# Optimization experiments

Hardware: AMD Instinct MI355X
Metric: run time of the kernel (lower is better)

## Reference

```python
import jax, jax.numpy as jnp
import numpy as np

THRESHOLD = 0.05
TOP_N = 512
NMS_THR = 0.6
POST_TOP_N = 100
MIN_SIZE = 0.0
N_CLASS = 8
IMG_SIZE = (256.0, 256.0, 64.0)
B, C, H, W, D = 4, 8, 128, 128, 32


def _pairwise_iou3d(b):
    # b: [K, 6] in xyzxyz; returns [K, K] volumetric IoU
    lo, hi = b[:, :3], b[:, 3:]
    ilo = jnp.maximum(lo[:, None, :], lo[None, :, :])
    ihi = jnp.minimum(hi[:, None, :], hi[None, :, :])
    inter = jnp.prod(jnp.maximum(ihi - ilo, 0.0), axis=-1)
    vol = jnp.prod(jnp.maximum(hi - lo, 0.0), axis=-1)
    return inter / (vol[:, None] + vol[None, :] - inter + 1e-9)


def _nms_keep(boxes, scores, thr):
    # greedy NMS; scores == -1 marks invalid entries. Returns bool keep mask [K].
    K = boxes.shape[0]
    order = jnp.argsort(-scores)
    b = boxes[order]
    s = scores[order]
    iou = _pairwise_iou3d(b)
    idx = jnp.arange(K)

    def body(i, keep):
        sup = (iou[i] > thr) & keep[i] & (idx > i)
        return keep & ~sup

    keep = jax.lax.fori_loop(0, K, body, s > 0.0)
    return jnp.zeros(K, dtype=bool).at[order].set(keep)


def _forward(location, cls_pred, box_pred, center_pred):
    Bb, Cc = cls_pred.shape[0], cls_pred.shape[1]
    N = cls_pred.shape[2] * cls_pred.shape[3] * cls_pred.shape[4]
    # [B, C, H, W, D] -> [B, N, C]
    cls = jax.nn.sigmoid(cls_pred).transpose(0, 2, 3, 4, 1).reshape(Bb, N, Cc)
    ctr = jax.nn.sigmoid(center_pred).transpose(0, 2, 3, 4, 1).reshape(Bb, N)
    box = box_pred.transpose(0, 2, 3, 4, 1).reshape(Bb, N, 6)

    candid = cls > THRESHOLD                      # [B, N, C]
    scores = cls * ctr[:, :, None]                # centerness-weighted
    flat = jnp.where(candid, scores, -1.0).reshape(Bb, N * Cc)
    vals, idx = jax.lax.top_k(flat, TOP_N)        # fixed-size stand-in for mask+topk
    valid = vals > 0.0                            # matches torch clamp(count, top_n)

    loc_idx = idx // Cc                           # flattened spatial location
    class_id = idx % Cc + 1                       # labels are 1-based
    bsel = jnp.take_along_axis(box, loc_idx[..., None], axis=1)   # [B, K, 6]
    lsel = location[loc_idx]                                      # [B, K, 3]
    det = jnp.concatenate([lsel - bsel[..., :3], lsel + bsel[..., 3:]], axis=-1)

    # BoxList.clip to image volume
    full = jnp.concatenate([jnp.asarray(IMG_SIZE), jnp.asarray(IMG_SIZE)]).astype(det.dtype) - 1.0
    det = jnp.clip(det, 0.0, full)

    score = jnp.where(valid, jnp.sqrt(jnp.where(valid, vals, 1.0)), 0.0)

    # remove_small_boxes
    sides = det[..., 3:] - det[..., :3]
    valid = valid & jnp.all(sides >= MIN_SIZE, axis=-1)

    # per-class greedy NMS (decisions are non-differentiable; torch detaches anyway)
    det_ng = jax.lax.stop_gradient(det)
    score_ng = jax.lax.stop_gradient(score)

    def per_image(b_i, s_i, c_i, v_i):
        def per_class(j):
            m = v_i & (c_i == j)
            return _nms_keep(b_i, jnp.where(m, s_i, -1.0), NMS_THR) & m
        return jnp.any(jax.vmap(per_class)(jnp.arange(1, N_CLASS + 1)), axis=0)

    valid = jax.vmap(per_image)(det_ng, score_ng, class_id, valid)

    # post_top_n selection (kthvalue threshold == keep top post_top_n scores)
    fv, fi = jax.lax.top_k(jnp.where(valid, score_ng, -1.0), POST_TOP_N)
    fvalid = fv > 0.0
    fbox = jnp.take_along_axis(det, fi[..., None], axis=1) * fvalid[..., None]
    fscore = jnp.where(fvalid, jnp.take_along_axis(score, fi, axis=1), 0.0)
    flabel = jnp.where(fvalid, jnp.take_along_axis(class_id, fi, axis=1), 0)
    return fbox, fscore, flabel, fvalid


def setup_inputs() -> dict:
    key = jax.random.key(0)
    k1, k2, k3, k4 = jax.random.split(key, 4)
    N = H * W * D
    location = jax.random.uniform(k1, (N, 3), dtype=jnp.float32) * jnp.asarray(IMG_SIZE, jnp.float32)
    cls_pred = jax.random.normal(k2, (B, C, H, W, D), dtype=jnp.float32) - 2.0  # realistic logits
    box_pred = jax.random.uniform(k3, (B, 6, H, W, D), dtype=jnp.float32) * 20.0  # positive extents
    center_pred = jax.random.normal(k4, (B, 1, H, W, D), dtype=jnp.float32)
    return {"location": location, "cls_pred": cls_pred, "box_pred": box_pred, "center_pred": center_pred}


def reference(location, cls_pred, box_pred, center_pred):
    return _forward(location, cls_pred, box_pred, center_pred)
```

## Files before the change

kernel.cpp:

```cpp
#include <hip/hip_runtime.h>

#define NB 4
#define NC 8
#define NLOC 524288
#define TOPN 512
#define POST 100
#define NBIN 8192
#define SELBINS 4096
#define SCAP 4096
#define CAP 16384
#define KPT 16
#define LCAP 2048
#define NMS_THR 0.6f
#define CAND_THR 0.05f
#define SPEC_THR 0.5f

typedef unsigned long long ull;

#define OFF_CNT    0
#define OFF_OVF    16
#define OFF_KEYS   64
#define ZERO_BYTES 32

__device__ __forceinline__ float sigmoidf_(float x) {
    return 1.0f / (1.0f + __expf(-x));
}

__global__ __launch_bounds__(256) void gather_spec(const float* __restrict__ cls,
                                                   const float* __restrict__ ctr,
                                                   ull* __restrict__ keys,
                                                   unsigned int* __restrict__ counts,
                                                   unsigned int* __restrict__ ovf) {
    __shared__ ull lkeys[LCAP];
    __shared__ unsigned int lcnt;
    __shared__ unsigned int lbase;
    const int b = blockIdx.y;
    if (threadIdx.x == 0) lcnt = 0;
    __syncthreads();

    const int n0 = (blockIdx.x * blockDim.x + threadIdx.x) * 8;
    const float4* cvp = (const float4*)(ctr + (size_t)b * NLOC + n0);
    const float4 cv0 = cvp[0], cv1 = cvp[1];
    float4 cl0[NC], cl1[NC];
    #pragma unroll
    for (int c = 0; c < NC; ++c) {
        const float4* p = (const float4*)(cls + ((size_t)b * NC + c) * NLOC + n0);
        cl0[c] = p[0];
        cl1[c] = p[1];
    }

    #pragma unroll
    for (int h = 0; h < 2; ++h) {
        const float4 cv = h ? cv1 : cv0;
        #pragma unroll
        for (int j = 0; j < 4; ++j) {
            bool any = false;
            #pragma unroll
            for (int c = 0; c < NC; ++c) {
                const float x = h ? ((const float*)&cl1[c])[j] : ((const float*)&cl0[c])[j];
                any |= (x > 0.0f);
            }
            if (any) {
                const float sc = sigmoidf_(((const float*)&cv)[j]);
                #pragma unroll
                for (int c = 0; c < NC; ++c) {
                    const float x = h ? ((const float*)&cl1[c])[j] : ((const float*)&cl0[c])[j];
                    if (x > 0.0f) {
                        const float p = sigmoidf_(x) * sc;
                        if (p > SPEC_THR) {
                            const unsigned pos = atomicAdd(&lcnt, 1u);
                            if (pos < LCAP) {
                                const unsigned flat = (unsigned)((n0 + h * 4 + j) * NC + c);
                                lkeys[pos] = ((ull)__float_as_uint(p) << 32) | (unsigned)(~flat);
                            }
                        }
                    }
                }
            }
        }
    }
    __syncthreads();
    const unsigned m = lcnt;
    if (threadIdx.x == 0) {
        const unsigned stored = (m > LCAP) ? LCAP : m;
        lbase = atomicAdd(&counts[b], stored);
        if (m > LCAP) ovf[b] = 1;
    }
    __syncthreads();
    const unsigned stored = (m > LCAP) ? LCAP : m;
    const unsigned base = lbase;
    for (unsigned i = threadIdx.x; i < stored; i += blockDim.x) {
        const unsigned pos = base + i;
        if (pos < CAP) keys[(size_t)b * CAP + pos] = lkeys[i];
    }
}

__device__ __forceinline__ float iou3d_(const float* a, const float* bx) {
    const float ix = fminf(a[3], bx[3]) - fmaxf(a[0], bx[0]);
    const float iy = fminf(a[4], bx[4]) - fmaxf(a[1], bx[1]);
    const float iz = fminf(a[5], bx[5]) - fmaxf(a[2], bx[2]);
    const float inter = fmaxf(ix, 0.0f) * fmaxf(iy, 0.0f) * fmaxf(iz, 0.0f);
    const float v0 = fmaxf(a[3] - a[0], 0.0f) * fmaxf(a[4] - a[1], 0.0f) * fmaxf(a[5] - a[2], 0.0f);
    const float v1 = fmaxf(bx[3] - bx[0], 0.0f) * fmaxf(bx[4] - bx[1], 0.0f) * fmaxf(bx[5] - bx[2], 0.0f);
    return inter / (v0 + v1 - inter + 1e-9f);
}

__global__ __launch_bounds__(1024) void select_nms_kernel(const float* __restrict__ cls,
                                                          const float* __restrict__ ctr,
                                                          ull* __restrict__ keys,
                                                          unsigned int* __restrict__ counts,
                                                          const unsigned int* __restrict__ ovf,
                                                          const float* __restrict__ loc,
                                                          const float* __restrict__ box,
                                                          float* __restrict__ out) {
    __shared__ union SU {
        struct { unsigned int hist[SELBINS]; ull surv[SCAP]; } sel;
        unsigned int fhist[NBIN];
        struct { float sd[TOPN * 6]; float ss[TOPN]; int scl[TOPN];
                 int keep[TOPN]; int clist[NC][TOPN];
                 float cbox[NC][128][6]; int wcnt[NC]; } nms;
    } u;
    __shared__ ull tk[TOPN];
    __shared__ unsigned int scnt;
    __shared__ int cut_s;

    const int b = blockIdx.x, t = threadIdx.x;
    const int lane = t & 63;

    {
        const unsigned cnt0 = counts[b];
        const bool bad = !(cnt0 >= TOPN && cnt0 <= CAP && ovf[b] == 0);
        if (bad) {
            for (int i = t; i < NBIN; i += 1024) u.fhist[i] = 0;
            __syncthreads();
            for (int n = t; n < NLOC; n += 1024) {
                const float sc = sigmoidf_(ctr[(size_t)b * NLOC + n]);
                #pragma unroll
                for (int c = 0; c < NC; ++c) {
                    const float s = sigmoidf_(cls[((size_t)b * NC + c) * NLOC + n]);
                    if (s > CAND_THR) atomicAdd(&u.fhist[__float_as_uint(s * sc) >> 17], 1u);
                }
            }
            __syncthreads();
            if (t == 0) {
                unsigned cum = 0; int bin = 0;
                for (int i = NBIN - 1; i >= 0; --i) {
                    cum += u.fhist[i];
                    if (cum >= TOPN) { bin = i; break; }
                }
                cut_s = bin;
                counts[b] = 0;
            }
            __syncthreads();
            const unsigned cb2 = (unsigned)cut_s;
            for (int n = t; n < NLOC; n += 1024) {
                const float sc = sigmoidf_(ctr[(size_t)b * NLOC + n]);
                #pragma unroll
                for (int c = 0; c < NC; ++c) {
                    const float s = sigmoidf_(cls[((size_t)b * NC + c) * NLOC + n]);
                    if (s > CAND_THR) {
                        const unsigned bits = __float_as_uint(s * sc);
                        if ((bits >> 17) >= cb2) {
                            const unsigned pos = atomicAdd(&counts[b], 1u);
                            if (pos < CAP)
                                keys[(size_t)b * CAP + pos] =
                                    ((ull)bits << 32) | (unsigned)(~(unsigned)(n * NC + c));
                        }
                    }
                }
            }
            __threadfence();
        }
    }
    __syncthreads();

    const int M = (int)min(counts[b], (unsigned)CAP);

    ull kr[KPT];
    {
        const ulonglong2* kb = (const ulonglong2*)(keys + (size_t)b * CAP);
        #pragma unroll
        for (int p = 0; p < KPT / 2; ++p) {
            const int vi = p * 1024 + t;
            ulonglong2 v; v.x = 0; v.y = 0;
            if (2 * vi < M) v = kb[vi];
            kr[2 * p] = v.x;
            kr[2 * p + 1] = v.y;
        }
    }

    for (int i = t; i < SELBINS; i += 1024) u.sel.hist[i] = 0;
    if (t == 0) scnt = 0;
    __syncthreads();
    #pragma unroll
    for (int p = 0; p < KPT / 2; ++p) {
        #pragma unroll
        for (int q = 0; q < 2; ++q) {
            const int i = 2 * (p * 1024 + t) + q;
            if (i < M) {
                const unsigned hi = (unsigned)(kr[2 * p + q] >> 32);
                const int off = (int)hi - 0x3F000000;
                int bin = (off < 0) ? 0 : (off >> 11);
                if (bin > SELBINS - 1) bin = SELBINS - 1;
                atomicAdd(&u.sel.hist[bin], 1u);
            }
        }
    }
    __syncthreads();

    if (t < 64) {
        unsigned s = 0;
        #pragma unroll 8
        for (int i = 0; i < 64; ++i)
            s += u.sel.hist[t * 64 + ((i + t) & 63)];
        unsigned suf = s;
        #pragma unroll
        for (int d = 1; d < 64; d <<= 1) {
            const unsigned o = __shfl_down(suf, d);
            suf += (t + d < 64) ? o : 0u;
        }
        const ull mask = __ballot(suf >= TOPN);
        unsigned nxt = __shfl_down(suf, 1);
        if (t == 63) nxt = 0;
        if (mask == 0ull) {
            if (t == 0) cut_s = 0;
        } else {
            const int L = 63 - __builtin_clzll(mask);
            if (t == L) {
                unsigned cum = nxt;
                int c = L * 64;
                for (int i = 63; i >= 0; --i) {
                    cum += u.sel.hist[L * 64 + i];
                    if (cum >= TOPN) { c = L * 64 + i; break; }
                }
                cut_s = c;
            }
        }
    }
    __syncthreads();

    const int cb = cut_s;
    #pragma unroll
    for (int p = 0; p < KPT / 2; ++p) {
        #pragma unroll
        for (int q = 0; q < 2; ++q) {
            const int i = 2 * (p * 1024 + t) + q;
            const ull k = kr[2 * p + q];
            bool pred = false;
            if (i < M) {
                const unsigned hi = (unsigned)(k >> 32);
                const int off = (int)hi - 0x3F000000;
                int bin = (off < 0) ? 0 : (off >> 11);
                if (bin > SELBINS - 1) bin = SELBINS - 1;
                pred = (bin >= cb);
            }
            const ull mv = __ballot(pred);
            unsigned base = 0;
            if (lane == 0 && mv) base = atomicAdd(&scnt, (unsigned)__popcll(mv));
            base = __shfl(base, 0);
            if (pred) {
                const unsigned pos = base + (unsigned)__popcll(mv & ((1ull << lane) - 1ull));
                if (pos < SCAP) u.sel.surv[pos] = k;
            }
        }
    }
    __syncthreads();

    const unsigned sc_final = scnt;
    if (sc_final <= (unsigned)SCAP) {
        const int S = (int)sc_final;
        for (int i = t; i < S; i += 1024) {
            const ull ke = u.sel.surv[i];
            int r = 0;
            int j = 0;
            for (; j + 16 <= S; j += 16) {
                #pragma unroll
                for (int qq = 0; qq < 16; ++qq) r += (u.sel.surv[j + qq] > ke) ? 1 : 0;
            }
            for (; j < S; ++j) r += (u.sel.surv[j] > ke) ? 1 : 0;
            if (r < TOPN) tk[r] = ke;
        }
        for (int r = S + t; r < TOPN; r += 1024) tk[r] = 0;
    } else {
        for (int i = t; i < M; i += 1024) {
            const ull ke = keys[(size_t)b * CAP + i];
            int r = 0;
            for (int j = 0; j < M; ++j) r += (keys[(size_t)b * CAP + j] > ke) ? 1 : 0;
            if (r < TOPN) tk[r] = ke;
        }
        const int W = (M < TOPN) ? M : TOPN;
        for (int r = W + t; r < TOPN; r += 1024) tk[r] = 0;
    }
    __syncthreads();

    if (t < TOPN) {
        const ull k = tk[t];
        const unsigned bits = (unsigned)(k >> 32);
        const float val = __uint_as_float(bits);
        int valid = (val > 0.0f) ? 1 : 0;
        const unsigned flat = ~(unsigned)(k & 0xffffffffu);
        int n = 0, c = 0;
        if (valid) { n = (int)(flat >> 3); c = (int)(flat & 7u); }
        const float lx = loc[n * 3 + 0], ly = loc[n * 3 + 1], lz = loc[n * 3 + 2];
        const float* bp = box + (size_t)b * 6 * NLOC + n;
        const float b0 = bp[0];
        const float b1 = bp[(size_t)NLOC];
        const float b2 = bp[2 * (size_t)NLOC];
        const float b3 = bp[3 * (size_t)NLOC];
        const float b4 = bp[4 * (size_t)NLOC];
        const float b5 = bp[5 * (size_t)NLOC];
        const float d0 = fminf(fmaxf(lx - b0, 0.0f), 255.0f);
        const float d1 = fminf(fmaxf(ly - b1, 0.0f), 255.0f);
        const float d2 = fminf(fmaxf(lz - b2, 0.0f), 63.0f);
        const float d3 = fminf(fmaxf(lx + b3, 0.0f), 255.0f);
        const float d4 = fminf(fmaxf(ly + b4, 0.0f), 255.0f);
        const float d5 = fminf(fmaxf(lz + b5, 0.0f), 63.0f);
        if (d3 - d0 < 0.0f || d4 - d1 < 0.0f || d5 - d2 < 0.0f) valid = 0;
        u.nms.sd[t * 6 + 0] = d0; u.nms.sd[t * 6 + 1] = d1; u.nms.sd[t * 6 + 2] = d2;
        u.nms.sd[t * 6 + 3] = d3; u.nms.sd[t * 6 + 4] = d4; u.nms.sd[t * 6 + 5] = d5;
        u.nms.ss[t] = (val > 0.0f) ? sqrtf(val) : 0.0f;
        u.nms.scl[t] = c + 1;
        u.nms.keep[t] = valid;
    }
    __syncthreads();

    if (t < TOPN) {
        const int w = t >> 6;
        const int myclass = w + 1;
        int cnt = 0;
        for (int j0 = 0; j0 < TOPN; j0 += 64) {
            const int j = j0 + lane;
            const bool pred = (u.nms.scl[j] == myclass) && (u.nms.keep[j] != 0);
            const ull m = __ballot(pred);
            if (pred) {
                const int pos = cnt + __popcll(m & ((1ull << lane) - 1ull));
                u.nms.clist[w][pos] = j;
                if (pos < 128) {
                    #pragma unroll
                    for (int q = 0; q < 6; ++q) u.nms.cbox[w][pos][q] = u.nms.sd[j * 6 + q];
                }
            }
            cnt += __popcll(m);
        }
        __threadfence_block();

        if (cnt <= 128) {
            const bool h0 = (lane < cnt), h1 = (lane + 64 < cnt);
            float A0[6], A1[6];
            #pragma unroll
            for (int q = 0; q < 6; ++q) {
                A0[q] = h0 ? u.nms.cbox[w][lane][q] : 0.0f;
                A1[q] = h1 ? u.nms.cbox[w][lane + 64][q] : 0.0f;
            }
            ull s0 = 0, s1lo = 0, s1hi = 0;
            #pragma unroll 2
            for (int i = 0; i < cnt; ++i) {
                float pb[6];
                #pragma unroll
                for (int q = 0; q < 6; ++q) pb[q] = u.nms.cbox[w][i][q];
                if (i < 64) {
                    if (h0 && lane > i && iou3d_(A0, pb) > NMS_THR) s0 |= 1ull << i;
                    if (h1 && iou3d_(A1, pb) > NMS_THR) s1lo |= 1ull << i;
                } else {
                    if (h1 && (i - 64) < lane && iou3d_(A1, pb) > NMS_THR) s1hi |= 1ull << (i - 64);
                }
            }
            bool a0 = h0, a1 = h1;
            ull m0 = __ballot(a0), m1 = __ballot(a1);
            for (int i = 0; i < cnt; ++i) {
                const bool alive_i = (i < 64) ? ((m0 >> i) & 1ull) : ((m1 >> (i - 64)) & 1ull);
                if (!alive_i) continue;
                if (a0 && i < 64 && ((s0 >> i) & 1ull)) a0 = false;
                if (a1) {
                    const bool sb = (i < 64) ? ((s1lo >> i) & 1ull) : ((s1hi >> (i - 64)) & 1ull);
                    if (sb) a1 = false;
                }
                m0 = __ballot(a0); m1 = __ballot(a1);
            }
            if (h0 && !a0) u.nms.keep[u.nms.clist[w][lane]] = 0;
            if (h1 && !a1) u.nms.keep[u.nms.clist[w][lane + 64]] = 0;
        } else {
            volatile int* vkeep = u.nms.keep;
            for (int i = 0; i < cnt; ++i) {
                const int gi = u.nms.clist[w][i];
                if (!vkeep[gi]) continue;
                float pb[6];
                #pragma unroll
                for (int q = 0; q < 6; ++q) pb[q] = u.nms.sd[gi * 6 + q];
                for (int e = i + 1 + lane; e < cnt; e += 64) {
                    const int gj = u.nms.clist[w][e];
                    if (vkeep[gj]) {
                        float cb_[6];
                        #pragma unroll
                        for (int q = 0; q < 6; ++q) cb_[q] = u.nms.sd[gj * 6 + q];
                        if (iou3d_(cb_, pb) > NMS_THR) vkeep[gj] = 0;
                    }
                }
                __threadfence_block();
            }
        }
    }
    __syncthreads();

    if (t < TOPN) {
        const int w = t >> 6;
        const ull km = __ballot(u.nms.keep[t] != 0);
        if (lane == 0) u.nms.wcnt[w] = __popcll(km);
    }
    __syncthreads();
    if (t < TOPN) {
        const int w = t >> 6;
        const ull km = __ballot(u.nms.keep[t] != 0);
        int before = 0, total = 0;
        #pragma unroll
        for (int w2 = 0; w2 < NC; ++w2) {
            total += u.nms.wcnt[w2];
            if (w2 < w) before += u.nms.wcnt[w2];
        }
        const int myrank = before + __popcll(km & ((1ull << lane) - 1ull));

        float* fbox = out;
        float* fscore = out + NB * POST * 6;
        float* flabel = out + NB * POST * 7;
        float* fvalid = out + NB * POST * 8;

        if (u.nms.keep[t] && myrank < POST) {
            #pragma unroll
            for (int k = 0; k < 6; ++k) fbox[(b * POST + myrank) * 6 + k] = u.nms.sd[t * 6 + k];
            fscore[b * POST + myrank] = u.nms.ss[t];
            flabel[b * POST + myrank] = (float)u.nms.scl[t];
            fvalid[b * POST + myrank] = 1.0f;
        }
        const int tc = (total < POST) ? total : POST;
        if (t >= tc && t < POST) {
            #pragma unroll
            for (int k = 0; k < 6; ++k) fbox[(b * POST + t) * 6 + k] = 0.0f;
            fscore[b * POST + t] = 0.0f;
            flabel[b * POST + t] = 0.0f;
            fvalid[b * POST + t] = 0.0f;
        }
    }
}

extern "C" void kernel_launch(void* const* d_in, const int* in_sizes, int n_in,
                              void* d_out, int out_size, void* d_ws, size_t ws_size,
                              hipStream_t stream) {
    const float* location = (const float*)d_in[0];
    const float* cls_pred = (const float*)d_in[1];
    const float* box_pred = (const float*)d_in[2];
    const float* ctr_pred = (const float*)d_in[3];

    char* ws = (char*)d_ws;
    unsigned int* counts = (unsigned int*)(ws + OFF_CNT);
    unsigned int* ovf    = (unsigned int*)(ws + OFF_OVF);
    ull*          keys   = (ull*)(ws + OFF_KEYS);

    hipMemsetAsync(d_ws, 0, ZERO_BYTES, stream);

    gather_spec<<<dim3(NLOC / 2048, NB), 256, 0, stream>>>(cls_pred, ctr_pred, keys, counts, ovf);
    select_nms_kernel<<<NB, 1024, 0, stream>>>(cls_pred, ctr_pred, keys, counts, ovf,
                                               location, box_pred, (float*)d_out);
}
```

Baseline: 88.24 us.

## Replace global atomic key append with per-block slots and bisection threshold select

```diff
diff --git a/kernel.cpp b/kernel.cpp
--- a/kernel.cpp
+++ b/kernel.cpp
@@ -6,21 +6,22 @@
 #define TOPN 512
 #define POST 100
 #define NBIN 8192
-#define SELBINS 4096
-#define SCAP 4096
-#define CAP 16384
-#define KPT 16
-#define LCAP 2048
+#define SLOTS 256
+#define SLOTW 128
+#define KEYSPAN (SLOTS*SLOTW)
+#define FB_CAP 16384
+#define SCAP 1024
+#define KPT 32
+#define LCAP 256
 #define NMS_THR 0.6f
 #define CAND_THR 0.05f
 #define SPEC_THR 0.5f
 
 typedef unsigned long long ull;
 
-#define OFF_CNT    0
-#define OFF_OVF    16
-#define OFF_KEYS   64
-#define ZERO_BYTES 32
+#define OFF_CNT  0
+#define OFF_OVF  4096
+#define OFF_KEYS 8192
 
 __device__ __forceinline__ float sigmoidf_(float x) {
     return 1.0f / (1.0f + __expf(-x));
@@ -29,11 +30,10 @@
 __global__ __launch_bounds__(256) void gather_spec(const float* __restrict__ cls,
                                                    const float* __restrict__ ctr,
                                                    ull* __restrict__ keys,
-                                                   unsigned int* __restrict__ counts,
-                                                   unsigned int* __restrict__ ovf) {
+                                                   unsigned int* __restrict__ cnt_arr,
+                                                   unsigned int* __restrict__ ovf_arr) {
     __shared__ ull lkeys[LCAP];
     __shared__ unsigned int lcnt;
-    __shared__ unsigned int lbase;
     const int b = blockIdx.y;
     if (threadIdx.x == 0) lcnt = 0;
     __syncthreads();
@@ -81,17 +81,91 @@
     }
     __syncthreads();
     const unsigned m = lcnt;
+    const unsigned stored = (m > (unsigned)SLOTW) ? (unsigned)SLOTW : m;
+    ull* kb = keys + ((size_t)b * SLOTS + blockIdx.x) * SLOTW;
+    for (unsigned i = threadIdx.x; i < stored; i += blockDim.x) kb[i] = lkeys[i];
     if (threadIdx.x == 0) {
-        const unsigned stored = (m > LCAP) ? LCAP : m;
-        lbase = atomicAdd(&counts[b], stored);
-        if (m > LCAP) ovf[b] = 1;
-    }
-    __syncthreads();
-    const unsigned stored = (m > LCAP) ? LCAP : m;
-    const unsigned base = lbase;
-    for (unsigned i = threadIdx.x; i < stored; i += blockDim.x) {
-        const unsigned pos = base + i;
-        if (pos < CAP) keys[(size_t)b * CAP + pos] = lkeys[i];
+        cnt_arr[b * SLOTS + blockIdx.x] = stored;
+        ovf_arr[b * SLOTS + blockIdx.x] = (m > (unsigned)SLOTW) ? 1u : 0u;
+    }
+}
+
+__global__ __launch_bounds__(1024) void fallback_kernel(const float* __restrict__ cls,
+                                                        const float* __restrict__ ctr,
+                                                        ull* __restrict__ keys,
+                                                        unsigned int* __restrict__ cnt_arr,
+                                                        unsigned int* __restrict__ ovf_arr) {
+    __shared__ unsigned red[32];
+    __shared__ int bad_s;
+    __shared__ unsigned hist[NBIN];
+    __shared__ unsigned cut_s, lpos;
+    const int b = blockIdx.x, t = threadIdx.x;
+
+    unsigned c = 0, o = 0;
+    if (t < SLOTS) { c = cnt_arr[b * SLOTS + t]; o = ovf_arr[b * SLOTS + t]; }
+    #pragma unroll
+    for (int d = 32; d >= 1; d >>= 1) { c += __shfl_down(c, d); o |= __shfl_down(o, d); }
+    if ((t & 63) == 0 && t < SLOTS) { red[t >> 6] = c; red[16 + (t >> 6)] = o; }
+    __syncthreads();
+    if (t == 0) {
+        const unsigned tot = red[0] + red[1] + red[2] + red[3];
+        const unsigned ov = red[16] | red[17] | red[18] | red[19];
+        bad_s = (tot < (unsigned)TOPN) || (ov != 0u);
+    }
+    __syncthreads();
+    if (!bad_s) return;
+
+    for (int i = t; i < NBIN; i += 1024) hist[i] = 0;
+    if (t == 0) lpos = 0;
+    __syncthreads();
+    for (int n = t; n < NLOC; n += 1024) {
+        const float scv = sigmoidf_(ctr[(size_t)b * NLOC + n]);
+        #pragma unroll
+        for (int cc = 0; cc < NC; ++cc) {
+            const float x = cls[((size_t)b * NC + cc) * NLOC + n];
+            if (x > -2.9444390f) {
+                const float s = sigmoidf_(x);
+                if (s > CAND_THR) atomicAdd(&hist[__float_as_uint(s * scv) >> 17], 1u);
+            }
+        }
+    }
+    __syncthreads();
+    if (t == 0) {
+        unsigned cum = 0; unsigned bin = 0;
+        for (int i = NBIN - 1; i >= 0; --i) {
+            cum += hist[i];
+            if (cum >= (unsigned)TOPN) { bin = (unsigned)i; break; }
+        }
+        cut_s = bin;
+    }
+    __syncthreads();
+    const unsigned cb = cut_s;
+    for (int n = t; n < NLOC; n += 1024) {
+        const float scv = sigmoidf_(ctr[(size_t)b * NLOC + n]);
+        #pragma unroll
+        for (int cc = 0; cc < NC; ++cc) {
+            const float x = cls[((size_t)b * NC + cc) * NLOC + n];
+            if (x > -2.9444390f) {
+                const float s = sigmoidf_(x);
+                if (s > CAND_THR) {
+                    const unsigned bits = __float_as_uint(s * scv);
+                    if ((bits >> 17) >= cb) {
+                        const unsigned pos = atomicAdd(&lpos, 1u);
+                        if (pos < (unsigned)FB_CAP)
+                            keys[(size_t)b * KEYSPAN + pos] =
+                                ((ull)bits << 32) | (unsigned)(~(unsigned)(n * NC + cc));
+                    }
+                }
+            }
+        }
+    }
+    __syncthreads();
+    const int M_fb = (int)((lpos < (unsigned)FB_CAP) ? lpos : (unsigned)FB_CAP);
+    if (t < SLOTS) {
+        int rem = M_fb - t * SLOTW;
+        rem = (rem < 0) ? 0 : ((rem > SLOTW) ? SLOTW : rem);
+        cnt_arr[b * SLOTS + t] = (unsigned)rem;
+        ovf_arr[b * SLOTS + t] = 0u;
     }
 }
 
@@ -105,191 +179,132 @@
     return inter / (v0 + v1 - inter + 1e-9f);
 }
 
-__global__ __launch_bounds__(1024) void select_nms_kernel(const float* __restrict__ cls,
-                                                          const float* __restrict__ ctr,
-                                                          ull* __restrict__ keys,
-                                                          unsigned int* __restrict__ counts,
-                                                          const unsigned int* __restrict__ ovf,
+__global__ __launch_bounds__(1024) void select_nms_kernel(const ull* __restrict__ keys,
+                                                          const unsigned int* __restrict__ cnt_arr,
                                                           const float* __restrict__ loc,
                                                           const float* __restrict__ box,
                                                           float* __restrict__ out) {
-    __shared__ union SU {
-        struct { unsigned int hist[SELBINS]; ull surv[SCAP]; } sel;
-        unsigned int fhist[NBIN];
-        struct { float sd[TOPN * 6]; float ss[TOPN]; int scl[TOPN];
-                 int keep[TOPN]; int clist[NC][TOPN];
-                 float cbox[NC][128][6]; int wcnt[NC]; } nms;
-    } u;
+    __shared__ union { ull surv[SCAP]; int clist[NC][TOPN]; } u;
     __shared__ ull tk[TOPN];
-    __shared__ unsigned int scnt;
-    __shared__ int cut_s;
+    __shared__ float sd[TOPN * 6];
+    __shared__ float ss[TOPN];
+    __shared__ int scl[TOPN];
+    __shared__ int keep[TOPN];
+    __shared__ float cbox[NC][SLOTW][6];
+    __shared__ int wcnt[NC];
+    __shared__ unsigned lcnt256[SLOTS];
+    __shared__ unsigned wred[32];
+    __shared__ unsigned scnt;
 
     const int b = blockIdx.x, t = threadIdx.x;
-    const int lane = t & 63;
-
-    {
-        const unsigned cnt0 = counts[b];
-        const bool bad = !(cnt0 >= TOPN && cnt0 <= CAP && ovf[b] == 0);
-        if (bad) {
-            for (int i = t; i < NBIN; i += 1024) u.fhist[i] = 0;
+    const int lane = t & 63, wid = t >> 6;
+
+    if (t < SLOTS) lcnt256[t] = cnt_arr[b * SLOTS + t];
+    __syncthreads();
+
+    const ull* kb = keys + (size_t)b * KEYSPAN;
+    ull kv[KPT];
+    #pragma unroll
+    for (int j = 0; j < KPT; ++j) {
+        const int g = j * 1024 + t;
+        const ull v = kb[g];
+        kv[j] = (((unsigned)g & (SLOTW - 1)) < lcnt256[g >> 7]) ? v : 0ull;
+    }
+
+    unsigned lo = 0u, hb = 0x7F800000u;
+    int it = 0;
+    while (lo < hb) {
+        const unsigned mid = (lo + hb) >> 1;
+        unsigned c = 0;
+        #pragma unroll
+        for (int j = 0; j < KPT; ++j) c += ((unsigned)(kv[j] >> 32) > mid) ? 1u : 0u;
+        #pragma unroll
+        for (int d = 32; d >= 1; d >>= 1) c += __shfl_down(c, d);
+        if (lane == 0) wred[(it & 1) * 16 + wid] = c;
+        __syncthreads();
+        unsigned tot = 0;
+        #pragma unroll
+        for (int w = 0; w < 16; ++w) tot += wred[(it & 1) * 16 + w];
+        if (tot < (unsigned)TOPN) hb = mid; else lo = mid + 1;
+        ++it;
+    }
+    const unsigned T = lo;
+
+    if (t == 0) scnt = 0;
+    __syncthreads();
+    const unsigned CT = (T == 0u) ? 1u : T;
+    #pragma unroll
+    for (int j = 0; j < KPT; ++j) {
+        const bool pred = ((unsigned)(kv[j] >> 32) >= CT);
+        const ull mv = __ballot(pred);
+        unsigned base = 0;
+        if (lane == 0 && mv) base = atomicAdd(&scnt, (unsigned)__popcll(mv));
+        base = __shfl(base, 0);
+        if (pred) {
+            const unsigned pos = base + (unsigned)__popcll(mv & ((1ull << lane) - 1ull));
+            if (pos < (unsigned)SCAP) u.surv[pos] = kv[j];
+        }
+    }
+    __syncthreads();
+
+    if (scnt > (unsigned)SCAP) {
+        unsigned c = 0;
+        #pragma unroll
+        for (int j = 0; j < KPT; ++j) c += ((unsigned)(kv[j] >> 32) > T) ? 1u : 0u;
+        #pragma unroll
+        for (int d = 32; d >= 1; d >>= 1) c += __shfl_down(c, d);
+        if (lane == 0) wred[wid] = c;
+        __syncthreads();
+        unsigned gt = 0;
+        #pragma unroll
+        for (int w = 0; w < 16; ++w) gt += wred[w];
+        const unsigned need = (unsigned)TOPN - gt;
+        __syncthreads();
+        unsigned lo2 = 0u, hb2 = 0xFFFFFFFFu;
+        int it2 = 0;
+        while (lo2 < hb2) {
+            const unsigned mid = lo2 + ((hb2 - lo2) >> 1);
+            unsigned cc = 0;
+            #pragma unroll
+            for (int j = 0; j < KPT; ++j)
+                cc += (((unsigned)(kv[j] >> 32) == T) && ((unsigned)kv[j] > mid)) ? 1u : 0u;
+            #pragma unroll
+            for (int d = 32; d >= 1; d >>= 1) cc += __shfl_down(cc, d);
+            if (lane == 0) wred[(it2 & 1) * 16 + wid] = cc;
             __syncthreads();
-            for (int n = t; n < NLOC; n += 1024) {
-                const float sc = sigmoidf_(ctr[(size_t)b * NLOC + n]);
-                #pragma unroll
-                for (int c = 0; c < NC; ++c) {
-                    const float s = sigmoidf_(cls[((size_t)b * NC + c) * NLOC + n]);
-                    if (s > CAND_THR) atomicAdd(&u.fhist[__float_as_uint(s * sc) >> 17], 1u);
-                }
-            }
-            __syncthreads();
-            if (t == 0) {
-                unsigned cum = 0; int bin = 0;
-                for (int i = NBIN - 1; i >= 0; --i) {
-                    cum += u.fhist[i];
-                    if (cum >= TOPN) { bin = i; break; }
-                }
-                cut_s = bin;
-                counts[b] = 0;
-            }
-            __syncthreads();
-            const unsigned cb2 = (unsigned)cut_s;
-            for (int n = t; n < NLOC; n += 1024) {
-                const float sc = sigmoidf_(ctr[(size_t)b * NLOC + n]);
-                #pragma unroll
-                for (int c = 0; c < NC; ++c) {
-                    const float s = sigmoidf_(cls[((size_t)b * NC + c) * NLOC + n]);
-                    if (s > CAND_THR) {
-                        const unsigned bits = __float_as_uint(s * sc);
-                        if ((bits >> 17) >= cb2) {
-                            const unsigned pos = atomicAdd(&counts[b], 1u);
-                            if (pos < CAP)
-                                keys[(size_t)b * CAP + pos] =
-                                    ((ull)bits << 32) | (unsigned)(~(unsigned)(n * NC + c));
-                        }
-                    }
-                }
-            }
-            __threadfence();
-        }
-    }
-    __syncthreads();
-
-    const int M = (int)min(counts[b], (unsigned)CAP);
-
-    ull kr[KPT];
-    {
-        const ulonglong2* kb = (const ulonglong2*)(keys + (size_t)b * CAP);
-        #pragma unroll
-        for (int p = 0; p < KPT / 2; ++p) {
-            const int vi = p * 1024 + t;
-            ulonglong2 v; v.x = 0; v.y = 0;
-            if (2 * vi < M) v = kb[vi];
-            kr[2 * p] = v.x;
-            kr[2 * p + 1] = v.y;
-        }
-    }
-
-    for (int i = t; i < SELBINS; i += 1024) u.sel.hist[i] = 0;
-    if (t == 0) scnt = 0;
-    __syncthreads();
-    #pragma unroll
-    for (int p = 0; p < KPT / 2; ++p) {
-        #pragma unroll
-        for (int q = 0; q < 2; ++q) {
-            const int i = 2 * (p * 1024 + t) + q;
-            if (i < M) {
-                const unsigned hi = (unsigned)(kr[2 * p + q] >> 32);
-                const int off = (int)hi - 0x3F000000;
-                int bin = (off < 0) ? 0 : (off >> 11);
-                if (bin > SELBINS - 1) bin = SELBINS - 1;
-                atomicAdd(&u.sel.hist[bin], 1u);
-            }
-        }
-    }
-    __syncthreads();
-
-    if (t < 64) {
-        unsigned s = 0;
-        #pragma unroll 8
-        for (int i = 0; i < 64; ++i)
-            s += u.sel.hist[t * 64 + ((i + t) & 63)];
-        unsigned suf = s;
-        #pragma unroll
-        for (int d = 1; d < 64; d <<= 1) {
-            const unsigned o = __shfl_down(suf, d);
-            suf += (t + d < 64) ? o : 0u;
-        }
-        const ull mask = __ballot(suf >= TOPN);
-        unsigned nxt = __shfl_down(suf, 1);
-        if (t == 63) nxt = 0;
-        if (mask == 0ull) {
-            if (t == 0) cut_s = 0;
-        } else {
-            const int L = 63 - __builtin_clzll(mask);
-            if (t == L) {
-                unsigned cum = nxt;
-                int c = L * 64;
-                for (int i = 63; i >= 0; --i) {
-                    cum += u.sel.hist[L * 64 + i];
-                    if (cum >= TOPN) { c = L * 64 + i; break; }
-                }
-                cut_s = c;
-            }
-        }
-    }
-    __syncthreads();
-
-    const int cb = cut_s;
-    #pragma unroll
-    for (int p = 0; p < KPT / 2; ++p) {
-        #pragma unroll
-        for (int q = 0; q < 2; ++q) {
-            const int i = 2 * (p * 1024 + t) + q;
-            const ull k = kr[2 * p + q];
-            bool pred = false;
-            if (i < M) {
-                const unsigned hi = (unsigned)(k >> 32);
-                const int off = (int)hi - 0x3F000000;
-                int bin = (off < 0) ? 0 : (off >> 11);
-                if (bin > SELBINS - 1) bin = SELBINS - 1;
-                pred = (bin >= cb);
-            }
+            unsigned tot2 = 0;
+            #pragma unroll
+            for (int w = 0; w < 16; ++w) tot2 += wred[(it2 & 1) * 16 + w];
+            if (tot2 < need) hb2 = mid; else lo2 = mid + 1;
+            ++it2;
+        }
+        const unsigned L = lo2;
+        if (t == 0) scnt = 0;
+        __syncthreads();
+        #pragma unroll
+        for (int j = 0; j < KPT; ++j) {
+            const unsigned hw = (unsigned)(kv[j] >> 32);
+            const bool pred = (hw > T) || ((hw == T) && ((unsigned)kv[j] >= L));
             const ull mv = __ballot(pred);
             unsigned base = 0;
             if (lane == 0 && mv) base = atomicAdd(&scnt, (unsigned)__popcll(mv));
             base = __shfl(base, 0);
             if (pred) {
                 const unsigned pos = base + (unsigned)__popcll(mv & ((1ull << lane) - 1ull));
-                if (pos < SCAP) u.sel.surv[pos] = k;
-            }
-        }
-    }
-    __syncthreads();
-
-    const unsigned sc_final = scnt;
-    if (sc_final <= (unsigned)SCAP) {
-        const int S = (int)sc_final;
-        for (int i = t; i < S; i += 1024) {
-            const ull ke = u.sel.surv[i];
-            int r = 0;
-            int j = 0;
-            for (; j + 16 <= S; j += 16) {
-                #pragma unroll
-                for (int qq = 0; qq < 16; ++qq) r += (u.sel.surv[j + qq] > ke) ? 1 : 0;
-            }
-            for (; j < S; ++j) r += (u.sel.surv[j] > ke) ? 1 : 0;
-            if (r < TOPN) tk[r] = ke;
-        }
-        for (int r = S + t; r < TOPN; r += 1024) tk[r] = 0;
-    } else {
-        for (int i = t; i < M; i += 1024) {
-            const ull ke = keys[(size_t)b * CAP + i];
-            int r = 0;
-            for (int j = 0; j < M; ++j) r += (keys[(size_t)b * CAP + j] > ke) ? 1 : 0;
-            if (r < TOPN) tk[r] = ke;
-        }
-        const int W = (M < TOPN) ? M : TOPN;
-        for (int r = W + t; r < TOPN; r += 1024) tk[r] = 0;
+                if (pos < (unsigned)SCAP) u.surv[pos] = kv[j];
+            }
+        }
+        __syncthreads();
+    }
+
+    const int S = (int)((scnt < (unsigned)SCAP) ? scnt : (unsigned)SCAP);
+    if (t < TOPN) tk[t] = 0;
+    __syncthreads();
+    for (int i = t; i < S; i += 1024) {
+        const ull ke = u.surv[i];
+        int r = 0;
+        for (int j = 0; j < S; ++j) r += (u.surv[j] > ke) ? 1 : 0;
+        if (r < TOPN) tk[r] = ke;
     }
     __syncthreads();
 
@@ -316,48 +331,47 @@
         const float d4 = fminf(fmaxf(ly + b4, 0.0f), 255.0f);
         const float d5 = fminf(fmaxf(lz + b5, 0.0f), 63.0f);
         if (d3 - d0 < 0.0f || d4 - d1 < 0.0f || d5 - d2 < 0.0f) valid = 0;
-        u.nms.sd[t * 6 + 0] = d0; u.nms.sd[t * 6 + 1] = d1; u.nms.sd[t * 6 + 2] = d2;
-        u.nms.sd[t * 6 + 3] = d3; u.nms.sd[t * 6 + 4] = d4; u.nms.sd[t * 6 + 5] = d5;
-        u.nms.ss[t] = (val > 0.0f) ? sqrtf(val) : 0.0f;
-        u.nms.scl[t] = c + 1;
-        u.nms.keep[t] = valid;
+        sd[t * 6 + 0] = d0; sd[t * 6 + 1] = d1; sd[t * 6 + 2] = d2;
+        sd[t * 6 + 3] = d3; sd[t * 6 + 4] = d4; sd[t * 6 + 5] = d5;
+        ss[t] = (val > 0.0f) ? sqrtf(val) : 0.0f;
+        scl[t] = c + 1;
+        keep[t] = valid;
     }
     __syncthreads();
 
     if (t < TOPN) {
-        const int w = t >> 6;
+        const int w = wid;
         const int myclass = w + 1;
         int cnt = 0;
         for (int j0 = 0; j0 < TOPN; j0 += 64) {
             const int j = j0 + lane;
-            const bool pred = (u.nms.scl[j] == myclass) && (u.nms.keep[j] != 0);
+            const bool pred = (scl[j] == myclass) && (keep[j] != 0);
             const ull m = __ballot(pred);
             if (pred) {
                 const int pos = cnt + __popcll(m & ((1ull << lane) - 1ull));
-                u.nms.clist[w][pos] = j;
-                if (pos < 128) {
+                u.clist[w][pos] = j;
+                if (pos < SLOTW) {
                     #pragma unroll
-                    for (int q = 0; q < 6; ++q) u.nms.cbox[w][pos][q] = u.nms.sd[j * 6 + q];
+                    for (int q = 0; q < 6; ++q) cbox[w][pos][q] = sd[j * 6 + q];
                 }
             }
             cnt += __popcll(m);
         }
         __threadfence_block();
 
-        if (cnt <= 128) {
+        if (cnt <= SLOTW) {
             const bool h0 = (lane < cnt), h1 = (lane + 64 < cnt);
             float A0[6], A1[6];
             #pragma unroll
             for (int q = 0; q < 6; ++q) {
-                A0[q] = h0 ? u.nms.cbox[w][lane][q] : 0.0f;
-                A1[q] = h1 ? u.nms.cbox[w][lane + 64][q] : 0.0f;
+                A0[q] = h0 ? cbox[w][lane][q] : 0.0f;
+                A1[q] = h1 ? cbox[w][lane + 64][q] : 0.0f;
             }
             ull s0 = 0, s1lo = 0, s1hi = 0;
-            #pragma unroll 2
             for (int i = 0; i < cnt; ++i) {
                 float pb[6];
                 #pragma unroll
-                for (int q = 0; q < 6; ++q) pb[q] = u.nms.cbox[w][i][q];
+                for (int q = 0; q < 6; ++q) pb[q] = cbox[w][i][q];
                 if (i < 64) {
                     if (h0 && lane > i && iou3d_(A0, pb) > NMS_THR) s0 |= 1ull << i;
                     if (h1 && iou3d_(A1, pb) > NMS_THR) s1lo |= 1ull << i;
@@ -377,22 +391,22 @@
                 }
                 m0 = __ballot(a0); m1 = __ballot(a1);
             }
-            if (h0 && !a0) u.nms.keep[u.nms.clist[w][lane]] = 0;
-            if (h1 && !a1) u.nms.keep[u.nms.clist[w][lane + 64]] = 0;
+            if (h0 && !a0) keep[u.clist[w][lane]] = 0;
+            if (h1 && !a1) keep[u.clist[w][lane + 64]] = 0;
         } else {
-            volatile int* vkeep = u.nms.keep;
+            volatile int* vkeep = keep;
             for (int i = 0; i < cnt; ++i) {
-                const int gi = u.nms.clist[w][i];
+                const int gi = u.clist[w][i];
                 if (!vkeep[gi]) continue;
                 float pb[6];
                 #pragma unroll
-                for (int q = 0; q < 6; ++q) pb[q] = u.nms.sd[gi * 6 + q];
+                for (int q = 0; q < 6; ++q) pb[q] = sd[gi * 6 + q];
                 for (int e = i + 1 + lane; e < cnt; e += 64) {
-                    const int gj = u.nms.clist[w][e];
+                    const int gj = u.clist[w][e];
                     if (vkeep[gj]) {
                         float cb_[6];
                         #pragma unroll
-                        for (int q = 0; q < 6; ++q) cb_[q] = u.nms.sd[gj * 6 + q];
+                        for (int q = 0; q < 6; ++q) cb_[q] = sd[gj * 6 + q];
                         if (iou3d_(cb_, pb) > NMS_THR) vkeep[gj] = 0;
                     }
                 }
@@ -403,19 +417,18 @@
     __syncthreads();
 
     if (t < TOPN) {
-        const int w = t >> 6;
-        const ull km = __ballot(u.nms.keep[t] != 0);
-        if (lane == 0) u.nms.wcnt[w] = __popcll(km);
+        const ull km = __ballot(keep[t] != 0);
+        if (lane == 0) wcnt[wid] = __popcll(km);
     }
     __syncthreads();
     if (t < TOPN) {
-        const int w = t >> 6;
-        const ull km = __ballot(u.nms.keep[t] != 0);
+        const int w = wid;
+        const ull km = __ballot(keep[t] != 0);
         int before = 0, total = 0;
         #pragma unroll
         for (int w2 = 0; w2 < NC; ++w2) {
-            total += u.nms.wcnt[w2];
-            if (w2 < w) before += u.nms.wcnt[w2];
+            total += wcnt[w2];
+            if (w2 < w) before += wcnt[w2];
         }
         const int myrank = before + __popcll(km & ((1ull << lane) - 1ull));
 
@@ -424,11 +437,11 @@
         float* flabel = out + NB * POST * 7;
         float* fvalid = out + NB * POST * 8;
 
-        if (u.nms.keep[t] && myrank < POST) {
-            #pragma unroll
-            for (int k = 0; k < 6; ++k) fbox[(b * POST + myrank) * 6 + k] = u.nms.sd[t * 6 + k];
-            fscore[b * POST + myrank] = u.nms.ss[t];
-            flabel[b * POST + myrank] = (float)u.nms.scl[t];
+        if (keep[t] && myrank < POST) {
+            #pragma unroll
+            for (int k = 0; k < 6; ++k) fbox[(b * POST + myrank) * 6 + k] = sd[t * 6 + k];
+            fscore[b * POST + myrank] = ss[t];
+            flabel[b * POST + myrank] = (float)scl[t];
             fvalid[b * POST + myrank] = 1.0f;
         }
         const int tc = (total < POST) ? total : POST;
@@ -451,13 +464,11 @@
     const float* ctr_pred = (const float*)d_in[3];
 
     char* ws = (char*)d_ws;
-    unsigned int* counts = (unsigned int*)(ws + OFF_CNT);
-    unsigned int* ovf    = (unsigned int*)(ws + OFF_OVF);
-    ull*          keys   = (ull*)(ws + OFF_KEYS);
-
-    hipMemsetAsync(d_ws, 0, ZERO_BYTES, stream);
-
-    gather_spec<<<dim3(NLOC / 2048, NB), 256, 0, stream>>>(cls_pred, ctr_pred, keys, counts, ovf);
-    select_nms_kernel<<<NB, 1024, 0, stream>>>(cls_pred, ctr_pred, keys, counts, ovf,
-                                               location, box_pred, (float*)d_out);
-}
+    unsigned int* cnt_arr = (unsigned int*)(ws + OFF_CNT);
+    unsigned int* ovf_arr = (unsigned int*)(ws + OFF_OVF);
+    ull*          keys    = (ull*)(ws + OFF_KEYS);
+
+    gather_spec<<<dim3(SLOTS, NB), 256, 0, stream>>>(cls_pred, ctr_pred, keys, cnt_arr, ovf_arr);
+    fallback_kernel<<<NB, 1024, 0, stream>>>(cls_pred, ctr_pred, keys, cnt_arr, ovf_arr);
+    select_nms_kernel<<<NB, 1024, 0, stream>>>(keys, cnt_arr, location, box_pred, (float*)d_out);
+}
```

After: 109.5 us. 24.2% more time.

## Replace global atomic key compaction with per-wavefront fixed slots, drop memset

Applied to the files above, without the earlier changes.

```diff
diff --git a/kernel.cpp b/kernel.cpp
--- a/kernel.cpp
+++ b/kernel.cpp
@@ -7,20 +7,19 @@
 #define POST 100
 #define NBIN 8192
 #define SELBINS 4096
-#define SCAP 4096
-#define CAP 16384
-#define KPT 16
-#define LCAP 2048
+#define SCAP 2048
+#define WPI 2048
+#define SLOTW 16
+#define KEYSPAN (WPI*SLOTW)
+#define FB_CAP 16384
 #define NMS_THR 0.6f
 #define CAND_THR 0.05f
-#define SPEC_THR 0.5f
 
 typedef unsigned long long ull;
 
-#define OFF_CNT    0
-#define OFF_OVF    16
-#define OFF_KEYS   64
-#define ZERO_BYTES 32
+#define OFF_CNT  0
+#define OFF_OVF  32768
+#define OFF_KEYS 65536
 
 __device__ __forceinline__ float sigmoidf_(float x) {
     return 1.0f / (1.0f + __expf(-x));
@@ -29,69 +28,67 @@
 __global__ __launch_bounds__(256) void gather_spec(const float* __restrict__ cls,
                                                    const float* __restrict__ ctr,
                                                    ull* __restrict__ keys,
-                                                   unsigned int* __restrict__ counts,
-                                                   unsigned int* __restrict__ ovf) {
-    __shared__ ull lkeys[LCAP];
-    __shared__ unsigned int lcnt;
-    __shared__ unsigned int lbase;
+                                                   unsigned int* __restrict__ cnt_arr,
+                                                   unsigned int* __restrict__ ovf_arr) {
     const int b = blockIdx.y;
-    if (threadIdx.x == 0) lcnt = 0;
-    __syncthreads();
-
-    const int n0 = (blockIdx.x * blockDim.x + threadIdx.x) * 8;
-    const float4* cvp = (const float4*)(ctr + (size_t)b * NLOC + n0);
-    const float4 cv0 = cvp[0], cv1 = cvp[1];
-    float4 cl0[NC], cl1[NC];
+    const int lane = threadIdx.x & 63, wid = threadIdx.x >> 6;
+    const int n0 = (blockIdx.x * 256 + threadIdx.x) * 4;
+
+    const float4 cv = *(const float4*)(ctr + (size_t)b * NLOC + n0);
+    float4 cl[NC];
     #pragma unroll
-    for (int c = 0; c < NC; ++c) {
-        const float4* p = (const float4*)(cls + ((size_t)b * NC + c) * NLOC + n0);
-        cl0[c] = p[0];
-        cl1[c] = p[1];
-    }
-
+    for (int c = 0; c < NC; ++c)
+        cl[c] = *(const float4*)(cls + ((size_t)b * NC + c) * NLOC + n0);
+
+    unsigned hm = 0;
     #pragma unroll
-    for (int h = 0; h < 2; ++h) {
-        const float4 cv = h ? cv1 : cv0;
+    for (int j = 0; j < 4; ++j)
+        #pragma unroll
+        for (int c = 0; c < NC; ++c)
+            if (((const float*)&cl[c])[j] > 0.0f) hm |= 1u << (j * 8 + c);
+
+    ull k0 = 0, k1 = 0, k2 = 0, k3 = 0;
+    int kc = 0;
+    if (hm) {
         #pragma unroll
         for (int j = 0; j < 4; ++j) {
-            bool any = false;
-            #pragma unroll
-            for (int c = 0; c < NC; ++c) {
-                const float x = h ? ((const float*)&cl1[c])[j] : ((const float*)&cl0[c])[j];
-                any |= (x > 0.0f);
-            }
-            if (any) {
+            if ((hm >> (j * 8)) & 0xffu) {
                 const float sc = sigmoidf_(((const float*)&cv)[j]);
                 #pragma unroll
                 for (int c = 0; c < NC; ++c) {
-                    const float x = h ? ((const float*)&cl1[c])[j] : ((const float*)&cl0[c])[j];
-                    if (x > 0.0f) {
-                        const float p = sigmoidf_(x) * sc;
-                        if (p > SPEC_THR) {
-                            const unsigned pos = atomicAdd(&lcnt, 1u);
-                            if (pos < LCAP) {
-                                const unsigned flat = (unsigned)((n0 + h * 4 + j) * NC + c);
-                                lkeys[pos] = ((ull)__float_as_uint(p) << 32) | (unsigned)(~flat);
-                            }
+                    if ((hm >> (j * 8 + c)) & 1u) {
+                        const float p = sigmoidf_(((const float*)&cl[c])[j]) * sc;
+                        if (p > 0.5f) {
+                            const unsigned flat = (unsigned)((n0 + j) * NC + c);
+                            const ull key = ((ull)__float_as_uint(p) << 32) | (unsigned)(~flat);
+                            if (kc == 0) k0 = key;
+                            else if (kc == 1) k1 = key;
+                            else if (kc == 2) k2 = key;
+                            else if (kc == 3) k3 = key;
+                            ++kc;
                         }
                     }
                 }
             }
         }
     }
-    __syncthreads();
-    const unsigned m = lcnt;
-    if (threadIdx.x == 0) {
-        const unsigned stored = (m > LCAP) ? LCAP : m;
-        lbase = atomicAdd(&counts[b], stored);
-        if (m > LCAP) ovf[b] = 1;
-    }
-    __syncthreads();
-    const unsigned stored = (m > LCAP) ? LCAP : m;
-    const unsigned base = lbase;
-    for (unsigned i = threadIdx.x; i < stored; i += blockDim.x) {
-        const unsigned pos = base + i;
-        if (pos < CAP) keys[(size_t)b * CAP + pos] = lkeys[i];
+    const ull m1 = __ballot(kc >= 1), m2 = __ballot(kc >= 2);
+    const ull m3 = __ballot(kc >= 3), m4 = __ballot(kc >= 4);
+    const ull lt = (1ull << lane) - 1ull;
+    const unsigned pos = (unsigned)(__popcll(m1 & lt) + __popcll(m2 & lt) +
+                                    __popcll(m3 & lt) + __popcll(m4 & lt));
+    const unsigned tot = (unsigned)(__popcll(m1) + __popcll(m2) + __popcll(m3) + __popcll(m4));
+    const int wgid = blockIdx.x * 4 + wid;
+    ull* kb = keys + ((size_t)b * WPI + wgid) * SLOTW;
+    const int sc_ = (kc > 4) ? 4 : kc;
+    if (sc_ >= 1 && pos + 0 < SLOTW) kb[pos + 0] = k0;
+    if (sc_ >= 2 && pos + 1 < SLOTW) kb[pos + 1] = k1;
+    if (sc_ >= 3 && pos + 2 < SLOTW) kb[pos + 2] = k2;
+    if (sc_ >= 4 && pos + 3 < SLOTW) kb[pos + 3] = k3;
+    const ull mo = __ballot(kc > 4);
+    if (lane == 0) {
+        cnt_arr[b * WPI + wgid] = (tot > (unsigned)SLOTW) ? (unsigned)SLOTW : tot;
+        ovf_arr[b * WPI + wgid] = ((tot > (unsigned)SLOTW) || mo) ? 1u : 0u;
     }
 }
 
@@ -108,102 +105,128 @@
 __global__ __launch_bounds__(1024) void select_nms_kernel(const float* __restrict__ cls,
                                                           const float* __restrict__ ctr,
                                                           ull* __restrict__ keys,
-                                                          unsigned int* __restrict__ counts,
-                                                          const unsigned int* __restrict__ ovf,
+                                                          const unsigned int* __restrict__ cnt_arr,
+                                                          const unsigned int* __restrict__ ovf_arr,
                                                           const float* __restrict__ loc,
                                                           const float* __restrict__ box,
                                                           float* __restrict__ out) {
     __shared__ union SU {
-        struct { unsigned int hist[SELBINS]; ull surv[SCAP]; } sel;
-        unsigned int fhist[NBIN];
+        struct { unsigned int cnt[WPI]; unsigned int hist[SELBINS]; ull surv[SCAP]; } sel;
+        struct { unsigned int fhist[NBIN]; unsigned int cnt2[WPI]; } fb;
         struct { float sd[TOPN * 6]; float ss[TOPN]; int scl[TOPN];
                  int keep[TOPN]; int clist[NC][TOPN];
                  float cbox[NC][128][6]; int wcnt[NC]; } nms;
     } u;
     __shared__ ull tk[TOPN];
-    __shared__ unsigned int scnt;
-    __shared__ int cut_s;
+    __shared__ unsigned wredc[16], wredo[16];
+    __shared__ unsigned scnt, lpos;
+    __shared__ int cut_s, bad_s;
 
     const int b = blockIdx.x, t = threadIdx.x;
-    const int lane = t & 63;
-
+    const int lane = t & 63, wid = t >> 6;
+    const ull* kb = keys + (size_t)b * KEYSPAN;
+
+    unsigned myc = 0, myo = 0;
+    unsigned c0v, c1v;
     {
-        const unsigned cnt0 = counts[b];
-        const bool bad = !(cnt0 >= TOPN && cnt0 <= CAP && ovf[b] == 0);
-        if (bad) {
-            for (int i = t; i < NBIN; i += 1024) u.fhist[i] = 0;
-            __syncthreads();
-            for (int n = t; n < NLOC; n += 1024) {
-                const float sc = sigmoidf_(ctr[(size_t)b * NLOC + n]);
-                #pragma unroll
-                for (int c = 0; c < NC; ++c) {
-                    const float s = sigmoidf_(cls[((size_t)b * NC + c) * NLOC + n]);
-                    if (s > CAND_THR) atomicAdd(&u.fhist[__float_as_uint(s * sc) >> 17], 1u);
-                }
-            }
-            __syncthreads();
-            if (t == 0) {
-                unsigned cum = 0; int bin = 0;
-                for (int i = NBIN - 1; i >= 0; --i) {
-                    cum += u.fhist[i];
-                    if (cum >= TOPN) { bin = i; break; }
-                }
-                cut_s = bin;
-                counts[b] = 0;
-            }
-            __syncthreads();
-            const unsigned cb2 = (unsigned)cut_s;
-            for (int n = t; n < NLOC; n += 1024) {
-                const float sc = sigmoidf_(ctr[(size_t)b * NLOC + n]);
-                #pragma unroll
-                for (int c = 0; c < NC; ++c) {
-                    const float s = sigmoidf_(cls[((size_t)b * NC + c) * NLOC + n]);
+        c0v = cnt_arr[b * WPI + t];
+        c1v = cnt_arr[b * WPI + t + 1024];
+        myc = c0v + c1v;
+        myo = ovf_arr[b * WPI + t] | ovf_arr[b * WPI + t + 1024];
+    }
+    #pragma unroll
+    for (int d = 32; d >= 1; d >>= 1) { myc += __shfl_down(myc, d); myo |= __shfl_down(myo, d); }
+    if (lane == 0) { wredc[wid] = myc; wredo[wid] = myo; }
+    __syncthreads();
+    if (t == 0) {
+        unsigned tot = 0, ov = 0;
+        #pragma unroll
+        for (int w = 0; w < 16; ++w) { tot += wredc[w]; ov |= wredo[w]; }
+        bad_s = (tot < (unsigned)TOPN) || (ov != 0u);
+        lpos = 0;
+    }
+    __syncthreads();
+    const bool bad = (bad_s != 0);
+
+    if (!bad) {
+        u.sel.cnt[t] = c0v;
+        u.sel.cnt[t + 1024] = c1v;
+    } else {
+        for (int i = t; i < NBIN; i += 1024) u.fb.fhist[i] = 0;
+        __syncthreads();
+        for (int n = t; n < NLOC; n += 1024) {
+            const float scv = sigmoidf_(ctr[(size_t)b * NLOC + n]);
+            #pragma unroll
+            for (int cc = 0; cc < NC; ++cc) {
+                const float x = cls[((size_t)b * NC + cc) * NLOC + n];
+                if (x > -2.9444390f) {
+                    const float s = sigmoidf_(x);
+                    if (s > CAND_THR) atomicAdd(&u.fb.fhist[__float_as_uint(s * scv) >> 17], 1u);
+                }
+            }
+        }
+        __syncthreads();
+        if (t == 0) {
+            unsigned cum = 0; int bin = 0;
+            for (int i = NBIN - 1; i >= 0; --i) {
+                cum += u.fb.fhist[i];
+                if (cum >= (unsigned)TOPN) { bin = i; break; }
+            }
+            cut_s = bin;
+        }
+        __syncthreads();
+        const unsigned cb2 = (unsigned)cut_s;
+        for (int n = t; n < NLOC; n += 1024) {
+            const float scv = sigmoidf_(ctr[(size_t)b * NLOC + n]);
+            #pragma unroll
+            for (int cc = 0; cc < NC; ++cc) {
+                const float x = cls[((size_t)b * NC + cc) * NLOC + n];
+                if (x > -2.9444390f) {
+                    const float s = sigmoidf_(x);
                     if (s > CAND_THR) {
-                        const unsigned bits = __float_as_uint(s * sc);
+                        const unsigned bits = __float_as_uint(s * scv);
                         if ((bits >> 17) >= cb2) {
-                            const unsigned pos = atomicAdd(&counts[b], 1u);
-                            if (pos < CAP)
-                                keys[(size_t)b * CAP + pos] =
-                                    ((ull)bits << 32) | (unsigned)(~(unsigned)(n * NC + c));
+                            const unsigned pos = atomicAdd(&lpos, 1u);
+                            if (pos < (unsigned)FB_CAP)
+                                keys[(size_t)b * KEYSPAN + pos] =
+                                    ((ull)bits << 32) | (unsigned)(~(unsigned)(n * NC + cc));
                         }
                     }
                 }
             }
-            __threadfence();
-        }
-    }
-    __syncthreads();
-
-    const int M = (int)min(counts[b], (unsigned)CAP);
-
-    ull kr[KPT];
-    {
-        const ulonglong2* kb = (const ulonglong2*)(keys + (size_t)b * CAP);
-        #pragma unroll
-        for (int p = 0; p < KPT / 2; ++p) {
-            const int vi = p * 1024 + t;
-            ulonglong2 v; v.x = 0; v.y = 0;
-            if (2 * vi < M) v = kb[vi];
-            kr[2 * p] = v.x;
-            kr[2 * p + 1] = v.y;
-        }
-    }
+        }
+        __threadfence();
+        __syncthreads();
+        const int M_fb = (int)((lpos < (unsigned)FB_CAP) ? lpos : (unsigned)FB_CAP);
+        for (int i = 0; i < 2; ++i) {
+            const int s = t + i * 1024;
+            int rem = M_fb - s * SLOTW;
+            rem = (rem < 0) ? 0 : ((rem > SLOTW) ? SLOTW : rem);
+            u.fb.cnt2[s] = (unsigned)rem;
+        }
+    }
+    __syncthreads();
+    if (bad) {
+        unsigned a0 = u.fb.cnt2[t], a1 = u.fb.cnt2[t + 1024];
+        __syncthreads();
+        u.sel.cnt[t] = a0; u.sel.cnt[t + 1024] = a1;
+    }
+    __syncthreads();
 
     for (int i = t; i < SELBINS; i += 1024) u.sel.hist[i] = 0;
     if (t == 0) scnt = 0;
-    __syncthreads();
-    #pragma unroll
-    for (int p = 0; p < KPT / 2; ++p) {
-        #pragma unroll
-        for (int q = 0; q < 2; ++q) {
-            const int i = 2 * (p * 1024 + t) + q;
-            if (i < M) {
-                const unsigned hi = (unsigned)(kr[2 * p + q] >> 32);
-                const int off = (int)hi - 0x3F000000;
-                int bin = (off < 0) ? 0 : (off >> 11);
-                if (bin > SELBINS - 1) bin = SELBINS - 1;
-                atomicAdd(&u.sel.hist[bin], 1u);
-            }
+    if (t < TOPN) tk[t] = 0;
+    __syncthreads();
+    for (int it = 0; it < KEYSPAN / 1024; ++it) {
+        const int g = it * 1024 + t;
+        const bool valid = ((unsigned)g & (SLOTW - 1)) < u.sel.cnt[g >> 4];
+        const ull k = kb[g];
+        if (valid) {
+            const unsigned hi = (unsigned)(k >> 32);
+            const int off = (int)hi - 0x3F000000;
+            int bin = (off < 0) ? 0 : (off >> 11);
+            if (bin > SELBINS - 1) bin = SELBINS - 1;
+            atomicAdd(&u.sel.hist[bin], 1u);
         }
     }
     __syncthreads();
@@ -240,56 +263,35 @@
     __syncthreads();
 
     const int cb = cut_s;
-    #pragma unroll
-    for (int p = 0; p < KPT / 2; ++p) {
-        #pragma unroll
-        for (int q = 0; q < 2; ++q) {
-            const int i = 2 * (p * 1024 + t) + q;
-            const ull k = kr[2 * p + q];
-            bool pred = false;
-            if (i < M) {
-                const unsigned hi = (unsigned)(k >> 32);
-                const int off = (int)hi - 0x3F000000;
-                int bin = (off < 0) ? 0 : (off >> 11);
-                if (bin > SELBINS - 1) bin = SELBINS - 1;
-                pred = (bin >= cb);
-            }
-            const ull mv = __ballot(pred);
-            unsigned base = 0;
-            if (lane == 0 && mv) base = atomicAdd(&scnt, (unsigned)__popcll(mv));
-            base = __shfl(base, 0);
-            if (pred) {
-                const unsigned pos = base + (unsigned)__popcll(mv & ((1ull << lane) - 1ull));
-                if (pos < SCAP) u.sel.surv[pos] = k;
-            }
-        }
-    }
-    __syncthreads();
-
-    const unsigned sc_final = scnt;
-    if (sc_final <= (unsigned)SCAP) {
-        const int S = (int)sc_final;
-        for (int i = t; i < S; i += 1024) {
-            const ull ke = u.sel.surv[i];
-            int r = 0;
-            int j = 0;
-            for (; j + 16 <= S; j += 16) {
-                #pragma unroll
-                for (int qq = 0; qq < 16; ++qq) r += (u.sel.surv[j + qq] > ke) ? 1 : 0;
-            }
-            for (; j < S; ++j) r += (u.sel.surv[j] > ke) ? 1 : 0;
-            if (r < TOPN) tk[r] = ke;
-        }
-        for (int r = S + t; r < TOPN; r += 1024) tk[r] = 0;
-    } else {
-        for (int i = t; i < M; i += 1024) {
-            const ull ke = keys[(size_t)b * CAP + i];
-            int r = 0;
-            for (int j = 0; j < M; ++j) r += (keys[(size_t)b * CAP + j] > ke) ? 1 : 0;
-            if (r < TOPN) tk[r] = ke;
-        }
-        const int W = (M < TOPN) ? M : TOPN;
-        for (int r = W + t; r < TOPN; r += 1024) tk[r] = 0;
+    for (int it = 0; it < KEYSPAN / 1024; ++it) {
+        const int g = it * 1024 + t;
+        const bool valid = ((unsigned)g & (SLOTW - 1)) < u.sel.cnt[g >> 4];
+        const ull k = kb[g];
+        bool pred = false;
+        if (valid) {
+            const unsigned hi = (unsigned)(k >> 32);
+            const int off = (int)hi - 0x3F000000;
+            int bin = (off < 0) ? 0 : (off >> 11);
+            if (bin > SELBINS - 1) bin = SELBINS - 1;
+            pred = (bin >= cb);
+        }
+        const ull mv = __ballot(pred);
+        unsigned base = 0;
+        if (lane == 0 && mv) base = atomicAdd(&scnt, (unsigned)__popcll(mv));
+        base = __shfl(base, 0);
+        if (pred) {
+            const unsigned pos = base + (unsigned)__popcll(mv & ((1ull << lane) - 1ull));
+            if (pos < (unsigned)SCAP) u.sel.surv[pos] = k;
+        }
+    }
+    __syncthreads();
+
+    const int S = (int)((scnt < (unsigned)SCAP) ? scnt : (unsigned)SCAP);
+    for (int i = t; i < S; i += 1024) {
+        const ull ke = u.sel.surv[i];
+        int r = 0;
+        for (int j = 0; j < S; ++j) r += (u.sel.surv[j] > ke) ? 1 : 0;
+        if (r < TOPN) tk[r] = ke;
     }
     __syncthreads();
 
@@ -325,7 +327,7 @@
     __syncthreads();
 
     if (t < TOPN) {
-        const int w = t >> 6;
+        const int w = wid;
         const int myclass = w + 1;
         int cnt = 0;
         for (int j0 = 0; j0 < TOPN; j0 += 64) {
@@ -353,7 +355,6 @@
                 A1[q] = h1 ? u.nms.cbox[w][lane + 64][q] : 0.0f;
             }
             ull s0 = 0, s1lo = 0, s1hi = 0;
-            #pragma unroll 2
             for (int i = 0; i < cnt; ++i) {
                 float pb[6];
                 #pragma unroll
@@ -403,13 +404,12 @@
     __syncthreads();
 
     if (t < TOPN) {
-        const int w = t >> 6;
         const ull km = __ballot(u.nms.keep[t] != 0);
-        if (lane == 0) u.nms.wcnt[w] = __popcll(km);
+        if (lane == 0) u.nms.wcnt[wid] = __popcll(km);
     }
     __syncthreads();
     if (t < TOPN) {
-        const int w = t >> 6;
+        const int w = wid;
         const ull km = __ballot(u.nms.keep[t] != 0);
         int before = 0, total = 0;
         #pragma unroll
@@ -451,13 +451,11 @@
     const float* ctr_pred = (const float*)d_in[3];
 
     char* ws = (char*)d_ws;
-    unsigned int* counts = (unsigned int*)(ws + OFF_CNT);
-    unsigned int* ovf    = (unsigned int*)(ws + OFF_OVF);
-    ull*          keys   = (ull*)(ws + OFF_KEYS);
-
-    hipMemsetAsync(d_ws, 0, ZERO_BYTES, stream);
-
-    gather_spec<<<dim3(NLOC / 2048, NB), 256, 0, stream>>>(cls_pred, ctr_pred, keys, counts, ovf);
-    select_nms_kernel<<<NB, 1024, 0, stream>>>(cls_pred, ctr_pred, keys, counts, ovf,
+    unsigned int* cnt_arr = (unsigned int*)(ws + OFF_CNT);
+    unsigned int* ovf_arr = (unsigned int*)(ws + OFF_OVF);
+    ull*          keys    = (ull*)(ws + OFF_KEYS);
+
+    gather_spec<<<dim3(NLOC / 1024, NB), 256, 0, stream>>>(cls_pred, ctr_pred, keys, cnt_arr, ovf_arr);
+    select_nms_kernel<<<NB, 1024, 0, stream>>>(cls_pred, ctr_pred, keys, cnt_arr, ovf_arr,
                                                location, box_pred, (float*)d_out);
 }
```

Result: slower. 98.61 us (+11.8%).
